# Performance work log

Hardware: AMD Instinct MI355X
Metric: run time of the kernel (lower is better)

The kernel has to match this reference:

```python
import jax, jax.numpy as jnp
import numpy as np

B = 2; R_PER = 512; R = B * R_PER; RM_PER = 128; RM = B * RM_PER
NUM_CLASSES = 81; C = 256
IMG_H = 800.0; IMG_W = 800.0
SCALES = (0.25, 0.125, 0.0625, 0.03125)  # FPN strides 4,8,16,32
REG_W = (10.0, 10.0, 5.0, 5.0)
LOG_1000_16 = 4.135166556742356  # math.log(1000/16)


def _prep(c, size):
    # torchvision roi_align (aligned=False) coordinate handling
    valid = (c > -1.0) & (c < size)
    c = jnp.clip(c, 0.0, size - 1.0)
    lo = jnp.clip(jnp.floor(c), 0.0, size - 2.0).astype(jnp.int32)
    frac = c - lo.astype(c.dtype)
    return lo, frac, valid


def roi_align(feat, boxes, b_idx, scale, out_size, sr=2):
    # feat [B,C,H,W], boxes [R,4] in image coords, b_idx [R] int
    _, Cn, H, W = feat.shape
    bb = boxes * scale
    x1, y1 = bb[:, 0], bb[:, 1]
    rw = jnp.maximum(bb[:, 2] - x1, 1.0)
    rh = jnp.maximum(bb[:, 3] - y1, 1.0)
    n = out_size * sr
    g = (jnp.arange(n, dtype=feat.dtype) + 0.5) / (sr * out_size)
    ys = y1[:, None] + rh[:, None] * g[None, :]  # [R,n]
    xs = x1[:, None] + rw[:, None] * g[None, :]
    y0, ly, yv = _prep(ys, H)
    x0, lx, xv = _prep(xs, W)
    bi = b_idx[:, None, None]
    yy = y0[:, :, None]; xx = x0[:, None, :]
    f00 = feat[bi, :, yy, xx]          # [R,n,n,C]
    f01 = feat[bi, :, yy, xx + 1]
    f10 = feat[bi, :, yy + 1, xx]
    f11 = feat[bi, :, yy + 1, xx + 1]
    ly_ = ly[:, :, None, None]; lx_ = lx[:, None, :, None]
    v = (f00 * (1 - ly_) * (1 - lx_) + f01 * (1 - ly_) * lx_
         + f10 * ly_ * (1 - lx_) + f11 * ly_ * lx_)
    mask = (yv[:, :, None] & xv[:, None, :]).astype(v.dtype)[..., None]
    v = v * mask
    Rn = boxes.shape[0]
    v = v.reshape(Rn, out_size, sr, out_size, sr, Cn).mean(axis=(2, 4))
    return jnp.transpose(v, (0, 3, 1, 2))  # [R,C,out,out]


def multiscale_roi_align(feats, boxes, b_idx, out_size):
    area = jnp.maximum(boxes[:, 2] - boxes[:, 0], 0.0) * jnp.maximum(boxes[:, 3] - boxes[:, 1], 0.0)
    lvl = jnp.clip(jnp.floor(4.0 + jnp.log2(jnp.sqrt(area) / 224.0 + 1e-6)), 2.0, 5.0).astype(jnp.int32) - 2
    out = 0.0
    for i, (f, s) in enumerate(zip(feats, SCALES)):
        out = out + roi_align(f, boxes, b_idx, s, out_size) * (lvl == i)[:, None, None, None].astype(f.dtype)
    return out


def decode_boxes(deltas, boxes):
    # deltas [R,K,4], boxes [R,4]
    wx, wy, ww, wh = REG_W
    w = boxes[:, 2] - boxes[:, 0]; h = boxes[:, 3] - boxes[:, 1]
    cx = boxes[:, 0] + 0.5 * w; cy = boxes[:, 1] + 0.5 * h
    dx = deltas[..., 0] / wx; dy = deltas[..., 1] / wy
    dw = jnp.minimum(deltas[..., 2] / ww, LOG_1000_16)
    dh = jnp.minimum(deltas[..., 3] / wh, LOG_1000_16)
    pcx = dx * w[:, None] + cx[:, None]; pcy = dy * h[:, None] + cy[:, None]
    pw = jnp.exp(dw) * w[:, None]; ph = jnp.exp(dh) * h[:, None]
    out = jnp.stack([pcx - 0.5 * pw, pcy - 0.5 * ph, pcx + 0.5 * pw, pcy + 0.5 * ph], axis=-1)
    hi = jnp.array([IMG_W, IMG_H, IMG_W, IMG_H], dtype=out.dtype)
    return jnp.clip(out, 0.0, hi)  # process_box clip-to-image


def conv3x3(x, w, b):
    y = jax.lax.conv_general_dilated(x, w, (1, 1), ((1, 1), (1, 1)),
                                     dimension_numbers=('NCHW', 'OIHW', 'NCHW'))
    return jax.nn.relu(y + b[None, :, None, None])


def _forward(feat0, feat1, feat2, feat3, proposals, fc1_w, fc1_b, fc2_w, fc2_b,
             cls_w, cls_b, bbox_w, bbox_b, mconv_w, mconv_b, deconv_w, deconv_b,
             mlogit_w, mlogit_b, batch_idx):
    feats = (feat0, feat1, feat2, feat3)
    # box branch
    bf = multiscale_roi_align(feats, proposals, batch_idx, 7).reshape(R, -1)  # [R, 256*49]
    x = jax.nn.relu(bf @ fc1_w.T + fc1_b)
    x = jax.nn.relu(x @ fc2_w.T + fc2_b)
    scores = jax.nn.softmax(x @ cls_w.T + cls_b, axis=-1)          # [R,81]
    deltas = (x @ bbox_w.T + bbox_b).reshape(R, NUM_CLASSES, 4)
    boxes = decode_boxes(deltas, proposals)                        # [R,81,4]
    # mask branch on top-of-list detections (RM_PER per image), box at argmax fg class
    idx_m = jnp.concatenate([jnp.arange(RM_PER), R_PER + jnp.arange(RM_PER)])
    labels = jnp.argmax(scores[idx_m, 1:], axis=-1) + 1            # [RM]
    mboxes = boxes[idx_m, labels]                                  # [RM,4]
    mf = multiscale_roi_align(feats, mboxes, batch_idx[idx_m], 14)  # [RM,256,14,14]
    for i in range(4):
        mf = conv3x3(mf, mconv_w[i], mconv_b[i])
    # ConvTranspose2d k=2 s=2 (non-overlapping) as einsum, PyTorch IOHW weights
    t = jnp.einsum('bcij,copq->boipjq', mf, deconv_w).reshape(RM, C, 28, 28)
    t = jax.nn.relu(t + deconv_b[None, :, None, None])
    ml = jnp.einsum('bchw,oc->bohw', t, mlogit_w) + mlogit_b[None, :, None, None]
    masks = jax.nn.sigmoid(ml[jnp.arange(RM), labels])             # [RM,28,28]
    return scores, boxes, masks


def setup_inputs() -> dict:
    key = jax.random.key(0)
    ks = jax.random.split(key, 16)
    rn = lambda i, shape, s=1.0: jax.random.normal(ks[i], shape, dtype=jnp.float32) * s
    feat0 = rn(0, (B, C, 200, 200))
    feat1 = rn(1, (B, C, 100, 100))
    feat2 = rn(2, (B, C, 50, 50))
    feat3 = rn(3, (B, C, 25, 25))
    u = jax.random.uniform(ks[4], (R, 4), dtype=jnp.float32)
    x1 = u[:, 0] * (IMG_W - 64.0); y1 = u[:, 1] * (IMG_H - 64.0)
    w = 16.0 + u[:, 2] * 300.0; h = 16.0 + u[:, 3] * 300.0
    proposals = jnp.stack([x1, y1, jnp.minimum(x1 + w, IMG_W), jnp.minimum(y1 + h, IMG_H)], axis=1)
    batch_idx = jnp.repeat(jnp.arange(B, dtype=jnp.int32), R_PER)
    return dict(
        feat0=feat0, feat1=feat1, feat2=feat2, feat3=feat3,
        proposals=proposals,
        fc1_w=rn(5, (1024, C * 49), 0.01), fc1_b=jnp.zeros(1024, jnp.float32),
        fc2_w=rn(6, (1024, 1024), 0.02), fc2_b=jnp.zeros(1024, jnp.float32),
        cls_w=rn(7, (NUM_CLASSES, 1024), 0.02), cls_b=jnp.zeros(NUM_CLASSES, jnp.float32),
        bbox_w=rn(8, (NUM_CLASSES * 4, 1024), 0.01), bbox_b=jnp.zeros(NUM_CLASSES * 4, jnp.float32),
        mconv_w=rn(9, (4, C, C, 3, 3), 0.03), mconv_b=jnp.zeros((4, C), jnp.float32),
        deconv_w=rn(10, (C, C, 2, 2), 0.06), deconv_b=jnp.zeros(C, jnp.float32),
        mlogit_w=rn(11, (NUM_CLASSES, C), 0.06), mlogit_b=jnp.zeros(NUM_CLASSES, jnp.float32),
        batch_idx=batch_idx,
    )


def reference(feat0, feat1, feat2, feat3, proposals, fc1_w, fc1_b, fc2_w, fc2_b,
              cls_w, cls_b, bbox_w, bbox_b, mconv_w, mconv_b, deconv_w, deconv_b,
              mlogit_w, mlogit_b, batch_idx):
    return _forward(feat0, feat1, feat2, feat3, proposals, fc1_w, fc1_b, fc2_w, fc2_b,
                    cls_w, cls_b, bbox_w, bbox_b, mconv_w, mconv_b, deconv_w, deconv_b,
                    mlogit_w, mlogit_b, batch_idx)
```

## Files before the change

kernel.cpp:

```cpp
#include <hip/hip_runtime.h>


#define NUM_CLASSES 81
#define CDIM 256
#define RTOT 1024
#define RMASK 256
#define LOG1000_16 4.135166556742356f

typedef _Float16 half8v __attribute__((ext_vector_type(8)));
typedef _Float16 half4v __attribute__((ext_vector_type(4)));
typedef float    float4v __attribute__((ext_vector_type(4)));
typedef float    float2a4 __attribute__((ext_vector_type(2), aligned(4)));

__device__ __forceinline__ void gload_lds16(const void* g, void* l) {
    __builtin_amdgcn_global_load_lds(
        (const __attribute__((address_space(1))) void*)g,
        (__attribute__((address_space(3))) void*)l, 16, 0, 0);
}

__global__ __launch_bounds__(256) void transpose_nhwc_kernel(
    const float* __restrict__ in, float* __restrict__ out, int H, int W)
{
    __shared__ float tile[64][65];
    int t = threadIdx.x;
    int xl = t & 63, cq = t >> 6;
    int x0 = blockIdx.x * 64;
    int y  = blockIdx.y;
    int b  = blockIdx.z >> 2;
    int c0 = (blockIdx.z & 3) * 64;

    const float* ip = in + (((size_t)(b*CDIM + c0))*H + y)*W + x0;
    if (x0 + xl < W) {
        #pragma unroll
        for (int i = 0; i < 16; ++i) {
            int cl = cq + i*4;
            tile[cl][xl] = ip[(size_t)cl*H*W + xl];
        }
    }
    __syncthreads();
    float* op = out + (((size_t)b*H + y)*W + x0)*CDIM + c0;
    #pragma unroll
    for (int i = 0; i < 16; ++i) {
        int xw = cq + i*4;
        if (x0 + xw < W)
            op[(size_t)xw*CDIM + xl] = tile[xl][xw];
    }
}

__device__ __forceinline__ void axis_taps(
    float start, float ext, int o, float invn, int N,
    float* wgt, int* idx)
{
    #pragma unroll
    for (int s = 0; s < 2; ++s) {
        int i = o*2 + s;
        float g = ((float)i + 0.5f) * invn;
        float c = start + ext*g;
        float mv = ((c > -1.f) && (c < (float)N)) ? 1.f : 0.f;
        float cl = fminf(fmaxf(c, 0.f), (float)(N-1));
        int   i0 = (int)fminf(floorf(cl), (float)(N-2));
        float l  = cl - (float)i0;
        wgt[s*2+0] = (1.f-l)*mv;
        wgt[s*2+1] = l*mv;
        idx[s*2+0] = i0;
        idx[s*2+1] = i0+1;
    }
}

__global__ __launch_bounds__(256) void roi_align7_nhwc_kernel(
    const float* __restrict__ fT0, const float* __restrict__ fT1,
    const float* __restrict__ fT2, const float* __restrict__ fT3,
    const float* __restrict__ props, const int* __restrict__ bidx,
    _Float16* __restrict__ bf_h, _Float16* __restrict__ bf_l)
{
    __shared__ _Float16 lh[256*49];
    __shared__ _Float16 ll[256*49];
    int r = blockIdx.x, t = threadIdx.x;
    int lane = t & 63, wv = t >> 6;

    float x1 = props[r*4+0], y1 = props[r*4+1];
    float x2 = props[r*4+2], y2 = props[r*4+3];
    float area = fmaxf(x2-x1, 0.f) * fmaxf(y2-y1, 0.f);
    float lf = floorf(4.f + log2f(sqrtf(area)/224.f + 1e-6f));
    lf = fminf(fmaxf(lf, 2.f), 5.f);
    int lvl = (int)lf - 2;

    const float* fT; int H, W; float scale;
    if (lvl == 0)      { fT = fT0; H = 200; W = 200; scale = 0.25f; }
    else if (lvl == 1) { fT = fT1; H = 100; W = 100; scale = 0.125f; }
    else if (lvl == 2) { fT = fT2; H = 50;  W = 50;  scale = 0.0625f; }
    else               { fT = fT3; H = 25;  W = 25;  scale = 0.03125f; }
    int b = bidx[r];
    const float* fb = fT + ((size_t)b*H*W)*CDIM + lane*4;

    float x1s = x1*scale, y1s = y1*scale;
    float rw = fmaxf(x2*scale - x1s, 1.f);
    float rh = fmaxf(y2*scale - y1s, 1.f);

    for (int p = wv; p < 49; p += 4) {
        int oy = p / 7, ox = p % 7;
        float uy[4]; int yr[4];
        axis_taps(y1s, rh, oy, 1.f/14.f, H, uy, yr);
        float wx[4]; int xc[4];
        axis_taps(x1s, rw, ox, 1.f/14.f, W, wx, xc);

        float a0 = 0.f, a1 = 0.f, a2 = 0.f, a3 = 0.f;
        #pragma unroll
        for (int a = 0; a < 4; ++a) {
            const float* rowp = fb + (size_t)(yr[a]*W)*CDIM;
            #pragma unroll
            for (int c2 = 0; c2 < 4; ++c2) {
                float w = uy[a]*wx[c2];
                float4v v = *(const float4v*)(rowp + xc[c2]*CDIM);
                a0 += w*v[0]; a1 += w*v[1]; a2 += w*v[2]; a3 += w*v[3];
            }
        }
        float av[4] = {a0, a1, a2, a3};
        #pragma unroll
        for (int e = 0; e < 4; ++e) {
            float vv = av[e]*0.25f;
            _Float16 h = (_Float16)vv;
            int c = lane*4 + e;
            lh[c*49 + p] = h;
            ll[c*49 + p] = (_Float16)((vv - (float)h)*2048.f);
        }
    }
    __syncthreads();
    size_t ob = (size_t)r*12544;
    for (int k = t; k < 12544; k += 256) {
        bf_h[ob + k] = lh[k];
        bf_l[ob + k] = ll[k];
    }
}

__global__ __launch_bounds__(256) void roi_align14_nhwc_kernel(
    const float* __restrict__ fT0, const float* __restrict__ fT1,
    const float* __restrict__ fT2, const float* __restrict__ fT3,
    const float* __restrict__ mboxes, const int* __restrict__ bidx,
    _Float16* __restrict__ outT)
{
    int mi = blockIdx.x, py = blockIdx.y;
    int t = threadIdx.x;
    int lane = t & 63, wv = t >> 6;

    float x1 = mboxes[mi*4+0], y1 = mboxes[mi*4+1];
    float x2 = mboxes[mi*4+2], y2 = mboxes[mi*4+3];
    float area = fmaxf(x2-x1, 0.f) * fmaxf(y2-y1, 0.f);
    float lf = floorf(4.f + log2f(sqrtf(area)/224.f + 1e-6f));
    lf = fminf(fmaxf(lf, 2.f), 5.f);
    int lvl = (int)lf - 2;

    const float* fT; int H, W; float scale;
    if (lvl == 0)      { fT = fT0; H = 200; W = 200; scale = 0.25f; }
    else if (lvl == 1) { fT = fT1; H = 100; W = 100; scale = 0.125f; }
    else if (lvl == 2) { fT = fT2; H = 50;  W = 50;  scale = 0.0625f; }
    else               { fT = fT3; H = 25;  W = 25;  scale = 0.03125f; }
    int ridx = (mi < 128) ? mi : mi + 384;
    int b = bidx[ridx];
    const float* fb = fT + ((size_t)b*H*W)*CDIM + lane*4;

    float x1s = x1*scale, y1s = y1*scale;
    float rw = fmaxf(x2*scale - x1s, 1.f);
    float rh = fmaxf(y2*scale - y1s, 1.f);

    for (int pp = wv; pp < 49; pp += 4) {
        int p = py*49 + pp;
        int oy = p / 14, ox = p % 14;
        float uy[4]; int yr[4];
        axis_taps(y1s, rh, oy, 1.f/28.f, H, uy, yr);
        float wx[4]; int xc[4];
        axis_taps(x1s, rw, ox, 1.f/28.f, W, wx, xc);

        float a0 = 0.f, a1 = 0.f, a2 = 0.f, a3 = 0.f;
        #pragma unroll
        for (int a = 0; a < 4; ++a) {
            const float* rowp = fb + (size_t)(yr[a]*W)*CDIM;
            #pragma unroll
            for (int c2 = 0; c2 < 4; ++c2) {
                float w = uy[a]*wx[c2];
                float4v v = *(const float4v*)(rowp + xc[c2]*CDIM);
                a0 += w*v[0]; a1 += w*v[1]; a2 += w*v[2]; a3 += w*v[3];
            }
        }
        half4v hv;
        hv[0] = (_Float16)(a0*0.25f);
        hv[1] = (_Float16)(a1*0.25f);
        hv[2] = (_Float16)(a2*0.25f);
        hv[3] = (_Float16)(a3*0.25f);
        *(half4v*)(outT + ((size_t)mi*196 + p)*CDIM + lane*4) = hv;
    }
}

__global__ __launch_bounds__(256) void roi_align7_kernel(
    const float* __restrict__ f0, const float* __restrict__ f1,
    const float* __restrict__ f2, const float* __restrict__ f3,
    const float* __restrict__ props, const int* __restrict__ bidx,
    _Float16* __restrict__ bf_h, _Float16* __restrict__ bf_l)
{
    int r  = blockIdx.x;
    int cg = blockIdx.y;
    int t = threadIdx.x;
    if (t >= 196) return;
    int p  = t % 49;
    int cl = t / 49;
    int oy = p / 7, ox = p % 7;

    float x1 = props[r*4+0], y1 = props[r*4+1];
    float x2 = props[r*4+2], y2 = props[r*4+3];
    float area = fmaxf(x2-x1, 0.f) * fmaxf(y2-y1, 0.f);
    float lf = floorf(4.f + log2f(sqrtf(area)/224.f + 1e-6f));
    lf = fminf(fmaxf(lf, 2.f), 5.f);
    int lvl = (int)lf - 2;

    const float* feat; int H, W; float scale;
    if (lvl == 0)      { feat = f0; H = 200; W = 200; scale = 0.25f; }
    else if (lvl == 1) { feat = f1; H = 100; W = 100; scale = 0.125f; }
    else if (lvl == 2) { feat = f2; H = 50;  W = 50;  scale = 0.0625f; }
    else               { feat = f3; H = 25;  W = 25;  scale = 0.03125f; }
    int b = bidx[r];

    float x1s = x1*scale, y1s = y1*scale;
    float rw = fmaxf(x2*scale - x1s, 1.f);
    float rh = fmaxf(y2*scale - y1s, 1.f);

    int   offs[4];
    float w00[4], w01[4], w10[4], w11[4];
    #pragma unroll
    for (int sy = 0; sy < 2; ++sy) {
        int iy = oy*2 + sy;
        float gy = ((float)iy + 0.5f) / 14.f;
        float yc = y1s + rh*gy;
        bool  yv = (yc > -1.f) && (yc < (float)H);
        float ycl = fminf(fmaxf(yc, 0.f), (float)(H-1));
        int   y0  = (int)fminf(floorf(ycl), (float)(H-2));
        float ly  = ycl - (float)y0;
        #pragma unroll
        for (int sx = 0; sx < 2; ++sx) {
            int ix = ox*2 + sx;
            float gx = ((float)ix + 0.5f) / 14.f;
            float xc = x1s + rw*gx;
            bool  xv = (xc > -1.f) && (xc < (float)W);
            float xcl = fminf(fmaxf(xc, 0.f), (float)(W-1));
            int   x0  = (int)fminf(floorf(xcl), (float)(W-2));
            float lx  = xcl - (float)x0;
            float m = (yv && xv) ? 1.f : 0.f;
            int s = sy*2 + sx;
            offs[s] = y0*W + x0;
            w00[s] = (1.f-ly)*(1.f-lx)*m;
            w01[s] = (1.f-ly)*lx*m;
            w10[s] = ly*(1.f-lx)*m;
            w11[s] = ly*lx*m;
        }
    }

    size_t HW = (size_t)H * W;
    #pragma unroll 4
    for (int k = 0; k < 16; ++k) {
        int c = cg*64 + cl + k*4;
        const float* fb = feat + ((size_t)b*CDIM + c) * HW;
        float acc = 0.f;
        #pragma unroll
        for (int s = 0; s < 4; ++s) {
            const float* q = fb + offs[s];
            float2a4 u = *(const float2a4*)q;
            float2a4 v = *(const float2a4*)(q + W);
            acc += w00[s]*u.x + w01[s]*u.y + w10[s]*v.x + w11[s]*v.y;
        }
        float v = acc * 0.25f;
        _Float16 h = (_Float16)v;
        size_t o = (size_t)r*12544 + c*49 + p;
        bf_h[o] = h;
        bf_l[o] = (_Float16)((v - (float)h) * 2048.f);
    }
}

template<int BMODE>
__global__ __launch_bounds__(256, 2) void gemm_fc2(
    const _Float16* __restrict__ Ah, const _Float16* __restrict__ Al,
    const float* __restrict__ B32,
    const _Float16* __restrict__ Bh16, const _Float16* __restrict__ Bl16,
    float* __restrict__ Cp, int K, int KS, int NS)
{
    __shared__ __align__(16) char smem[2*32768];

    int t = threadIdx.x;
    int lane = t & 63, wave = t >> 6;
    int wm = wave >> 1, wn = wave & 1;
    int ln = lane & 15, q = lane >> 4;

    int gx = gridDim.x, gy = gridDim.y;
    int lin = blockIdx.x + gx*(blockIdx.y + gy*blockIdx.z);
    int per = (gx*gy*(int)gridDim.z) >> 3;
    int nl  = (lin & 7)*per + (lin >> 3);
    int bn  = nl % gx;
    int tmp = nl / gx;
    int bm  = tmp % gy;
    int kz  = tmp / gy;

    size_t kbase = (size_t)kz * KS;
    int asub = lane >> 2;
    int achk = (lane & 3) ^ ((lane >> 3) & 3);

    const _Float16* Agh0 = Ah + (size_t)(bm*128 + wave*32 + asub)*K + kbase + achk*8;
    const _Float16* Agh1 = Agh0 + (size_t)16*K;
    const _Float16* Agl0 = Al + (size_t)(bm*128 + wave*32 + asub)*K + kbase + achk*8;
    const _Float16* Agl1 = Agl0 + (size_t)16*K;
    int adst0 = (wave*32 + 0)*32;
    int adst1 = (wave*32 + 16)*32;

    const _Float16 *Bgh0=nullptr, *Bgh1=nullptr, *Bgl0=nullptr, *Bgl1=nullptr;
    const float *Bg0=nullptr, *Bg1=nullptr, *Bg2=nullptr, *Bg3=nullptr;
    int fdst0 = 0;
    if constexpr (BMODE == 1) {
        Bgh0 = Bh16 + (size_t)(bn*128 + wave*32 + asub)*K + kbase + achk*8;
        Bgh1 = Bgh0 + (size_t)16*K;
        Bgl0 = Bl16 + (size_t)(bn*128 + wave*32 + asub)*K + kbase + achk*8;
        Bgl1 = Bgl0 + (size_t)16*K;
    } else {
        int br8  = lane >> 3;
        int bchk = (lane & 7) ^ br8;
        const float* base = B32 + (size_t)(bn*128 + wave*32 + br8)*K + kbase + bchk*4;
        Bg0 = base;
        Bg1 = base + (size_t)8*K;
        Bg2 = base + (size_t)16*K;
        Bg3 = base + (size_t)24*K;
        fdst0 = (wave*32)*32;
    }

    auto AhB = [&](int b){ return (_Float16*)(smem + b*32768); };
    auto AlB = [&](int b){ return (_Float16*)(smem + b*32768 + 8192); };
    auto BhB = [&](int b){ return (_Float16*)(smem + b*32768 + 16384); };
    auto BlB = [&](int b){ return (_Float16*)(smem + b*32768 + 24576); };
    auto BfB = [&](int b){ return (float*)   (smem + b*32768 + 16384); };

    auto dma = [&](int k0, int b) {
        gload_lds16(Agh0 + k0, AhB(b) + adst0);
        gload_lds16(Agh1 + k0, AhB(b) + adst1);
        gload_lds16(Agl0 + k0, AlB(b) + adst0);
        gload_lds16(Agl1 + k0, AlB(b) + adst1);
        if constexpr (BMODE == 1) {
            gload_lds16(Bgh0 + k0, BhB(b) + adst0);
            gload_lds16(Bgh1 + k0, BhB(b) + adst1);
            gload_lds16(Bgl0 + k0, BlB(b) + adst0);
            gload_lds16(Bgl1 + k0, BlB(b) + adst1);
        } else {
            gload_lds16(Bg0 + k0, BfB(b) + fdst0);
            gload_lds16(Bg1 + k0, BfB(b) + fdst0 + 8*32);
            gload_lds16(Bg2 + k0, BfB(b) + fdst0 + 16*32);
            gload_lds16(Bg3 + k0, BfB(b) + fdst0 + 24*32);
        }
    };

    float4v acc1[4][4], acc2[4][4];
    #pragma unroll
    for (int i = 0; i < 4; ++i)
        #pragma unroll
        for (int j = 0; j < 4; ++j) {
            acc1[i][j] = (float4v){0.f,0.f,0.f,0.f};
            acc2[i][j] = (float4v){0.f,0.f,0.f,0.f};
        }

    int cq = (q ^ ((ln >> 1) & 3)) * 8;

    auto compute = [&](int b) {
        const _Float16* ah = AhB(b);
        const _Float16* al = AlB(b);
        half8v afh[4], afl[4], bfh[4], bfl[4];
        #pragma unroll
        for (int i = 0; i < 4; ++i) {
            int ra = (wm*64 + i*16 + ln)*32 + cq;
            afh[i] = *(const half8v*)&ah[ra];
            afl[i] = *(const half8v*)&al[ra];
        }
        if constexpr (BMODE == 1) {
            const _Float16* bh = BhB(b);
            const _Float16* bl = BlB(b);
            #pragma unroll
            for (int j = 0; j < 4; ++j) {
                int rb = (wn*64 + j*16 + ln)*32 + cq;
                bfh[j] = *(const half8v*)&bh[rb];
                bfl[j] = *(const half8v*)&bl[rb];
            }
        } else {
            const float* bfp = BfB(b);
            #pragma unroll
            for (int j = 0; j < 4; ++j) {
                int row = wn*64 + j*16 + ln;
                int c0 = (q*2)   ^ (row & 7);
                int c1 = (q*2+1) ^ (row & 7);
                float4v f0 = *(const float4v*)&bfp[row*32 + c0*4];
                float4v f1 = *(const float4v*)&bfp[row*32 + c1*4];
                #pragma unroll
                for (int e = 0; e < 4; ++e) {
                    _Float16 h0 = (_Float16)f0[e];
                    bfh[j][e] = h0;
                    bfl[j][e] = (_Float16)((f0[e] - (float)h0) * 2048.f);
                    _Float16 h1 = (_Float16)f1[e];
                    bfh[j][4+e] = h1;
                    bfl[j][4+e] = (_Float16)((f1[e] - (float)h1) * 2048.f);
                }
            }
        }
        #pragma unroll
        for (int i = 0; i < 4; ++i) {
            #pragma unroll
            for (int j = 0; j < 4; ++j) {
                acc1[i][j] = __builtin_amdgcn_mfma_f32_16x16x32_f16(
                    afh[i], bfh[j], acc1[i][j], 0, 0, 0);
                acc2[i][j] = __builtin_amdgcn_mfma_f32_16x16x32_f16(
                    afh[i], bfl[j], acc2[i][j], 0, 0, 0);
                acc2[i][j] = __builtin_amdgcn_mfma_f32_16x16x32_f16(
                    afl[i], bfh[j], acc2[i][j], 0, 0, 0);
            }
        }
    };

    int NT = KS / 32;
    dma(0, 0);
    if (NT > 1) dma(32, 1);

    for (int tt = 0; tt < NT; ++tt) {
        if (tt < NT-1) asm volatile("s_waitcnt vmcnt(8)" ::: "memory");
        else           asm volatile("s_waitcnt vmcnt(0)" ::: "memory");
        __builtin_amdgcn_s_barrier();
        asm volatile("" ::: "memory");
        compute(tt & 1);
        asm volatile("" ::: "memory");
        __builtin_amdgcn_s_barrier();
        if (tt + 2 < NT) dma((tt+2)*32, tt & 1);
    }

    float* Cpz = Cp + (size_t)kz*1024*NS;
    #pragma unroll
    for (int i = 0; i < 4; ++i) {
        #pragma unroll
        for (int j = 0; j < 4; ++j) {
            int col = bn*128 + wn*64 + j*16 + ln;
            #pragma unroll
            for (int reg = 0; reg < 4; ++reg) {
                int row = bm*128 + wm*64 + i*16 + q*4 + reg;
                Cpz[(size_t)row*NS + col] =
                    acc1[i][j][reg] + acc2[i][j][reg] * (1.f/2048.f);
            }
        }
    }
}

__global__ __launch_bounds__(256) void fc_reduce_kernel(
    const float* __restrict__ Cp, const float* __restrict__ bias,
    float* __restrict__ out, _Float16* __restrict__ outh,
    _Float16* __restrict__ outl, int nparts, int ns4, int do_relu)
{
    int i = blockIdx.x*256 + threadIdx.x;
    const float4* p = (const float4*)Cp;
    int pstride = 1024*ns4;
    float sx = 0.f, sy = 0.f, sz = 0.f, sw = 0.f;
    for (int j = 0; j < nparts; ++j) {
        float4 s = p[i + j*pstride];
        sx += s.x; sy += s.y; sz += s.z; sw += s.w;
    }
    float4 b4 = ((const float4*)bias)[i & (ns4-1)];
    float4 v;
    v.x = sx + b4.x; v.y = sy + b4.y; v.z = sz + b4.z; v.w = sw + b4.w;
    if (do_relu) {
        v.x = fmaxf(v.x, 0.f); v.y = fmaxf(v.y, 0.f);
        v.z = fmaxf(v.z, 0.f); v.w = fmaxf(v.w, 0.f);
    }
    if (out) ((float4*)out)[i] = v;
    if (outh) {
        float vv[4] = {v.x, v.y, v.z, v.w};
        half4v hh, hl;
        #pragma unroll
        for (int c2 = 0; c2 < 4; ++c2) {
            _Float16 h = (_Float16)vv[c2];
            hh[c2] = h;
            hl[c2] = (_Float16)((vv[c2] - (float)h) * 2048.f);
        }
        ((half4v*)outh)[i] = hh;
        ((half4v*)outl)[i] = hl;
    }
}

__global__ __launch_bounds__(256) void repack_split_kernel(
    const float* __restrict__ w, _Float16* __restrict__ h,
    _Float16* __restrict__ l)
{
    int i = blockIdx.x*256 + threadIdx.x;
    float4 v = ((const float4*)w)[i];
    float vv[4] = {v.x, v.y, v.z, v.w};
    half4v hh, hl;
    #pragma unroll
    for (int c2 = 0; c2 < 4; ++c2) {
        _Float16 hj = (_Float16)vv[c2];
        hh[c2] = hj;
        hl[c2] = (_Float16)((vv[c2] - (float)hj) * 2048.f);
    }
    ((half4v*)h)[i] = hh;
    ((half4v*)l)[i] = hl;
}

__global__ __launch_bounds__(256) void repack_head_kernel(
    const float* __restrict__ cls_w, const float* __restrict__ cls_b,
    const float* __restrict__ bbox_w, const float* __restrict__ bbox_b,
    _Float16* __restrict__ Wcat_h, _Float16* __restrict__ Wcat_l,
    float* __restrict__ bcat)
{
    int i = blockIdx.x*256 + threadIdx.x;
    int row = i >> 10, col = i & 1023;
    float v = 0.f;
    if (row < 81) v = cls_w[row*1024 + col];
    else if (row < 405) v = bbox_w[(row-81)*1024 + col];
    _Float16 h = (_Float16)v;
    Wcat_h[i] = h;
    Wcat_l[i] = (_Float16)((v - (float)h) * 2048.f);
    if (i < 512) {
        float bv = 0.f;
        if (i < 81) bv = cls_b[i];
        else if (i < 405) bv = bbox_b[i-81];
        bcat[i] = bv;
    }
}

__global__ __launch_bounds__(128) void heads_finish_kernel(
    const float* __restrict__ L, const float* __restrict__ props,
    float* __restrict__ scores, float* __restrict__ boxes,
    int* __restrict__ labels, float* __restrict__ mboxes)
{
    __shared__ float lg[NUM_CLASSES];
    __shared__ float red[2];
    __shared__ int slab;
    int r = blockIdx.x, t = threadIdx.x;
    const float* Lr = L + (size_t)r*512;
    if (t < NUM_CLASSES) lg[t] = Lr[t];
    __syncthreads();
    if (t == 0) {
        float mx = lg[0];
        for (int j = 1; j < NUM_CLASSES; ++j) mx = fmaxf(mx, lg[j]);
        red[0] = mx;
    }
    __syncthreads();
    float mx = red[0];
    if (t < NUM_CLASSES) lg[t] = expf(lg[t] - mx);
    __syncthreads();
    if (t == 0) {
        float s = 0.f;
        int best = 1; float bv = lg[1];
        for (int j = 0; j < NUM_CLASSES; ++j) {
            s += lg[j];
            if (j >= 1 && lg[j] > bv) { bv = lg[j]; best = j; }
        }
        red[1] = 1.f/s;
        slab = best;
    }
    __syncthreads();
    if (t < NUM_CLASSES) scores[(size_t)r*NUM_CLASSES + t] = lg[t]*red[1];

    bool sel = (r < 128) || (r >= 512 && r < 640);
    int mi = (r < 128) ? r : r - 384;
    if (t == 0 && sel) labels[mi] = slab;

    if (t < NUM_CLASSES) {
        float px1 = props[r*4+0], py1 = props[r*4+1];
        float px2 = props[r*4+2], py2 = props[r*4+3];
        float pw = px2 - px1, ph = py2 - py1;
        float cx = px1 + 0.5f*pw, cy = py1 + 0.5f*ph;
        const float* dl = Lr + 81 + t*4;
        float d0 = dl[0] * 0.1f;
        float d1 = dl[1] * 0.1f;
        float d2 = fminf(dl[2] * 0.2f, LOG1000_16);
        float d3 = fminf(dl[3] * 0.2f, LOG1000_16);
        float pcx = d0*pw + cx, pcy = d1*ph + cy;
        float qw = expf(d2)*pw, qh = expf(d3)*ph;
        float b0 = fminf(fmaxf(pcx - 0.5f*qw, 0.f), 800.f);
        float b1 = fminf(fmaxf(pcy - 0.5f*qh, 0.f), 800.f);
        float b2 = fminf(fmaxf(pcx + 0.5f*qw, 0.f), 800.f);
        float b3 = fminf(fmaxf(pcy + 0.5f*qh, 0.f), 800.f);
        size_t ob = ((size_t)r*NUM_CLASSES + t)*4;
        boxes[ob+0] = b0; boxes[ob+1] = b1; boxes[ob+2] = b2; boxes[ob+3] = b3;
        if (sel && t == slab) {
            mboxes[mi*4+0] = b0; mboxes[mi*4+1] = b1;
            mboxes[mi*4+2] = b2; mboxes[mi*4+3] = b3;
        }
    }
}

__global__ __launch_bounds__(256) void roi_align14_kernel(
    const float* __restrict__ f0, const float* __restrict__ f1,
    const float* __restrict__ f2, const float* __restrict__ f3,
    const float* __restrict__ mboxes, const int* __restrict__ bidx,
    _Float16* __restrict__ outT)
{
    int mi = blockIdx.x;
    int cg = blockIdx.y;
    int t = threadIdx.x;
    if (t >= 196) return;
    int oy = t / 14, ox = t % 14;

    float x1 = mboxes[mi*4+0], y1 = mboxes[mi*4+1];
    float x2 = mboxes[mi*4+2], y2 = mboxes[mi*4+3];
    float area = fmaxf(x2-x1, 0.f) * fmaxf(y2-y1, 0.f);
    float lf = floorf(4.f + log2f(sqrtf(area)/224.f + 1e-6f));
    lf = fminf(fmaxf(lf, 2.f), 5.f);
    int lvl = (int)lf - 2;

    const float* feat; int H, W; float scale;
    if (lvl == 0)      { feat = f0; H = 200; W = 200; scale = 0.25f; }
    else if (lvl == 1) { feat = f1; H = 100; W = 100; scale = 0.125f; }
    else if (lvl == 2) { feat = f2; H = 50;  W = 50;  scale = 0.0625f; }
    else               { feat = f3; H = 25;  W = 25;  scale = 0.03125f; }
    int ridx = (mi < 128) ? mi : mi + 384;
    int b = bidx[ridx];

    float x1s = x1*scale, y1s = y1*scale;
    float rw = fmaxf(x2*scale - x1s, 1.f);
    float rh = fmaxf(y2*scale - y1s, 1.f);

    int   offs[4];
    float w00[4], w01[4], w10[4], w11[4];
    #pragma unroll
    for (int sy = 0; sy < 2; ++sy) {
        int iy = oy*2 + sy;
        float gy = ((float)iy + 0.5f) / 28.f;
        float yc = y1s + rh*gy;
        bool  yv = (yc > -1.f) && (yc < (float)H);
        float ycl = fminf(fmaxf(yc, 0.f), (float)(H-1));
        int   y0  = (int)fminf(floorf(ycl), (float)(H-2));
        float ly  = ycl - (float)y0;
        #pragma unroll
        for (int sx = 0; sx < 2; ++sx) {
            int ix = ox*2 + sx;
            float gx = ((float)ix + 0.5f) / 28.f;
            float xc = x1s + rw*gx;
            bool  xv = (xc > -1.f) && (xc < (float)W);
            float xcl = fminf(fmaxf(xc, 0.f), (float)(W-1));
            int   x0  = (int)fminf(floorf(xcl), (float)(W-2));
            float lx  = xcl - (float)x0;
            float m = (yv && xv) ? 1.f : 0.f;
            int s = sy*2 + sx;
            offs[s] = y0*W + x0;
            w00[s] = (1.f-ly)*(1.f-lx)*m;
            w01[s] = (1.f-ly)*lx*m;
            w10[s] = ly*(1.f-lx)*m;
            w11[s] = ly*lx*m;
        }
    }

    size_t HW = (size_t)H * W;
    _Float16* orow = outT + ((size_t)mi*196 + t)*CDIM + cg*32;
    const float* fbase = feat + ((size_t)b*CDIM + cg*32) * HW;
    #pragma unroll
    for (int c8 = 0; c8 < 32; c8 += 8) {
        half8v hv;
        #pragma unroll
        for (int cc = 0; cc < 8; ++cc) {
            const float* fb = fbase + (size_t)(c8+cc) * HW;
            float acc = 0.f;
            #pragma unroll
            for (int s = 0; s < 4; ++s) {
                const float* q = fb + offs[s];
                float2a4 u = *(const float2a4*)q;
                float2a4 v = *(const float2a4*)(q + W);
                acc += w00[s]*u.x + w01[s]*u.y + w10[s]*v.x + w11[s]*v.y;
            }
            hv[cc] = (_Float16)(acc * 0.25f);
        }
        *(half8v*)(orow + c8) = hv;
    }
}

__global__ __launch_bounds__(256) void repack_wts_kernel(
    const float* __restrict__ w, _Float16* __restrict__ Wr)
{
    int i = blockIdx.x*256 + threadIdx.x;
    int ci = i & 255;
    int rest = i >> 8;
    int co = rest & 255;
    int rest2 = rest >> 8;
    int tap = rest2 % 9;
    int l = rest2 / 9;
    Wr[i] = (_Float16)w[(((size_t)(l*256 + co)*256 + ci)*9) + tap];
}

__global__ __launch_bounds__(256) void repack_dw_kernel(
    const float* __restrict__ dw, _Float16* __restrict__ Wd)
{
    int i = blockIdx.x*256 + threadIdx.x;
    int n = i >> 8, k = i & 255;
    Wd[i] = (_Float16)dw[(size_t)k*1024 + n];
}

#define PSTR 40

__global__ __launch_bounds__(256, 2) void conv3x3_mfma_kernel(
    const _Float16* __restrict__ inT, const _Float16* __restrict__ Wr,
    const float* __restrict__ bias, _Float16* __restrict__ outT, int layer)
{
    __shared__ _Float16 lin[256*PSTR];

    int t = threadIdx.x;
    int lane = t & 63;
    int wave = t >> 6;
    int ln = lane & 15;
    int q  = lane >> 4;
    int q8 = q*8;
    int r  = blockIdx.x >> 1;
    int bc = blockIdx.x & 1;
    int co_w = bc*128 + wave*32;

    const _Float16* WrL = Wr + (size_t)layer*9*256*256;
    const _Float16* inR = inT + (size_t)r*196*256;

    for (int i = t; i < 256*PSTR; i += 256) lin[i] = (_Float16)0.f;

    float4v acc[13][2];
    #pragma unroll
    for (int nt = 0; nt < 13; ++nt) {
        acc[nt][0] = (float4v){0.f,0.f,0.f,0.f};
        acc[nt][1] = (float4v){0.f,0.f,0.f,0.f};
    }

    for (int ci0 = 0; ci0 < 256; ci0 += 32) {
        __syncthreads();
        for (int idx = t; idx < 784; idx += 256) {
            int p = idx >> 2, g = idx & 3;
            float4 v = *(const float4*)(inR + (size_t)p*256 + ci0 + g*8);
            int row = (p*37450) >> 19;
            int col = p - row*14;
            *(float4*)&lin[((row+1)*16 + (col+1))*PSTR + g*8] = v;
        }
        __syncthreads();

        half8v aw[9][2];
        #pragma unroll
        for (int tap = 0; tap < 9; ++tap) {
            #pragma unroll
            for (int u = 0; u < 2; ++u)
                aw[tap][u] = *(const half8v*)(
                    WrL + ((size_t)tap*256 + co_w + u*16 + ln)*256 + ci0 + q8);
        }

        #pragma unroll
        for (int nt = 0; nt < 13; ++nt) {
            int n = nt*16 + ln;
            int row = (n*37450) >> 19;
            int col = n - row*14;
            int pb = (n < 196) ? (row*16 + col) : 0;
            const _Float16* bp = &lin[pb*PSTR + q8];
            #pragma unroll
            for (int ky = 0; ky < 3; ++ky) {
                #pragma unroll
                for (int kx = 0; kx < 3; ++kx) {
                    half8v bv = *(const half8v*)(bp + (ky*16 + kx)*PSTR);
                    acc[nt][0] = __builtin_amdgcn_mfma_f32_16x16x32_f16(
                        aw[ky*3+kx][0], bv, acc[nt][0], 0, 0, 0);
                    acc[nt][1] = __builtin_amdgcn_mfma_f32_16x16x32_f16(
                        aw[ky*3+kx][1], bv, acc[nt][1], 0, 0, 0);
                }
            }
        }
    }

    #pragma unroll
    for (int u = 0; u < 2; ++u) {
        float4 bi = *(const float4*)&bias[layer*256 + co_w + u*16 + q*4];
        float bia[4] = {bi.x, bi.y, bi.z, bi.w};
        #pragma unroll
        for (int nt = 0; nt < 13; ++nt) {
            int n = nt*16 + ln;
            if (n < 196) {
                half4v hv;
                #pragma unroll
                for (int i = 0; i < 4; ++i)
                    hv[i] = (_Float16)fmaxf(acc[nt][u][i] + bia[i], 0.f);
                *(half4v*)(outT + ((size_t)r*196 + n)*256 + co_w + u*16 + q*4) = hv;
            }
        }
    }
}

#define DSTR 264

template<int NMT>
__device__ __forceinline__ void deconv_pass(
    const _Float16* actL, const _Float16* __restrict__ Wd,
    const float* __restrict__ db, const float* __restrict__ mlw,
    int lab, float (*sred)[4], int wv, int ln, int q, int px0)
{
    float P[NMT][4];
    #pragma unroll
    for (int mt = 0; mt < NMT; ++mt)
        #pragma unroll
        for (int r2 = 0; r2 < 4; ++r2) P[mt][r2] = 0.f;

    for (int c = 0; c < 8; ++c) {
        int n0 = wv*256 + c*32;
        float4v acc[NMT][2];
        #pragma unroll
        for (int mt = 0; mt < NMT; ++mt) {
            acc[mt][0] = (float4v){0.f,0.f,0.f,0.f};
            acc[mt][1] = (float4v){0.f,0.f,0.f,0.f};
        }
        #pragma unroll
        for (int k = 0; k < 8; ++k) {
            const _Float16* wp = Wd + ((size_t)(n0 + ln))*256 + k*32 + q*8;
            half8v b0 = *(const half8v*)wp;
            half8v b1 = *(const half8v*)(wp + 16*256);
            #pragma unroll
            for (int mt = 0; mt < NMT; ++mt) {
                half8v a = *(const half8v*)&actL[(mt*16 + ln)*DSTR + k*32 + q*8];
                acc[mt][0] = __builtin_amdgcn_mfma_f32_16x16x32_f16(
                    a, b0, acc[mt][0], 0, 0, 0);
                acc[mt][1] = __builtin_amdgcn_mfma_f32_16x16x32_f16(
                    a, b1, acc[mt][1], 0, 0, 0);
            }
        }
        #pragma unroll
        for (int j = 0; j < 2; ++j) {
            int n = n0 + j*16 + ln;
            int o = n >> 2;
            float bo = db[o];
            float wl = mlw[lab*256 + o];
            #pragma unroll
            for (int mt = 0; mt < NMT; ++mt)
                #pragma unroll
                for (int r2 = 0; r2 < 4; ++r2)
                    P[mt][r2] += fmaxf(acc[mt][j][r2] + bo, 0.f) * wl;
        }
    }
    #pragma unroll
    for (int mt = 0; mt < NMT; ++mt)
        #pragma unroll
        for (int r2 = 0; r2 < 4; ++r2) {
            float v = P[mt][r2];
            v += __shfl_xor(v, 4);
            v += __shfl_xor(v, 8);
            int px = px0 + mt*16 + q*4 + r2;
            if (ln < 4 && px < 196) atomicAdd(&sred[px][ln], v);
        }
}

__global__ __launch_bounds__(256, 1) void deconv_mask_mfma_kernel(
    const _Float16* __restrict__ mfT, const _Float16* __restrict__ Wd,
    const float* __restrict__ db, const float* __restrict__ mlw,
    const float* __restrict__ mlb, const int* __restrict__ labels,
    float* __restrict__ masks)
{
    __shared__ _Float16 act[112*DSTR];
    __shared__ float sred[196][4];
    int t = threadIdx.x;
    int lane = t & 63, wv = t >> 6, ln = lane & 15, q = lane >> 4;
    int mi = blockIdx.x;
    int lab = labels[mi];

    for (int i = t; i < 784; i += 256) ((float*)sred)[i] = 0.f;

    for (int idx = t; idx < 112*32; idx += 256) {
        int px = idx >> 5, g = idx & 31;
        *(float4*)&act[px*DSTR + g*8] =
            *(const float4*)(mfT + ((size_t)mi*196 + px)*256 + g*8);
    }
    __syncthreads();
    deconv_pass<7>(act, Wd, db, mlw, lab, sred, wv, ln, q, 0);
    __syncthreads();

    for (int idx = t; idx < 84*32; idx += 256) {
        int px = idx >> 5, g = idx & 31;
        *(float4*)&act[px*DSTR + g*8] =
            *(const float4*)(mfT + ((size_t)mi*196 + 112 + px)*256 + g*8);
    }
    __syncthreads();
    deconv_pass<6>(act, Wd, db, mlw, lab, sred, wv, ln, q, 112);
    __syncthreads();

    if (t < 196) {
        float bl = mlb[lab];
        int i2 = t / 14, j2 = t % 14;
        #pragma unroll
        for (int pq = 0; pq < 4; ++pq) {
            float s = sred[t][pq] + bl;
            int h = 2*i2 + (pq >> 1), w2 = 2*j2 + (pq & 1);
            masks[(size_t)mi*784 + h*28 + w2] = 1.f/(1.f + expf(-s));
        }
    }
}

extern "C" void kernel_launch(void* const* d_in, const int* in_sizes, int n_in,
                              void* d_out, int out_size, void* d_ws, size_t ws_size,
                              hipStream_t stream) {
    const float* f0      = (const float*)d_in[0];
    const float* f1      = (const float*)d_in[1];
    const float* f2      = (const float*)d_in[2];
    const float* f3      = (const float*)d_in[3];
    const float* props   = (const float*)d_in[4];
    const float* fc1_w   = (const float*)d_in[5];
    const float* fc1_b   = (const float*)d_in[6];
    const float* fc2_w   = (const float*)d_in[7];
    const float* fc2_b   = (const float*)d_in[8];
    const float* cls_w   = (const float*)d_in[9];
    const float* cls_b   = (const float*)d_in[10];
    const float* bbox_w  = (const float*)d_in[11];
    const float* bbox_b  = (const float*)d_in[12];
    const float* mconv_w = (const float*)d_in[13];
    const float* mconv_b = (const float*)d_in[14];
    const float* dconv_w = (const float*)d_in[15];
    const float* dconv_b = (const float*)d_in[16];
    const float* mlog_w  = (const float*)d_in[17];
    const float* mlog_b  = (const float*)d_in[18];
    const int*   bidx    = (const int*)d_in[19];

    char* wsb = (char*)d_ws;
    _Float16* bf_h = (_Float16*)wsb;
    _Float16* bf_l = (_Float16*)(wsb + 25690112);
    _Float16* fc2h = (_Float16*)wsb;
    _Float16* fc2l = (_Float16*)(wsb + 2097152);
    _Float16* bufA = (_Float16*)wsb;
    _Float16* bufB = (_Float16*)(wsb + 25690112);
    _Float16* x1h  = (_Float16*)(wsb + 51380224);
    _Float16* x1l  = (_Float16*)(wsb + 53477376);
    _Float16* x2h  = (_Float16*)(wsb + 55574528);
    _Float16* x2l  = (_Float16*)(wsb + 57671680);
    int*      labels = (int*)(wsb + 59768832);
    float*    mboxes = (float*)(wsb + 59772928);
    float*    Cp     = (float*)(wsb + 59781120);
    _Float16* Wr     = (_Float16*)(wsb + 59781120);
    _Float16* Wd     = (_Float16*)(wsb + 64499712);
    _Float16* Wcat_h = (_Float16*)(wsb + 76558336);
    _Float16* Wcat_l = (_Float16*)(wsb + 77606912);
    float*    bcat   = (float*)(wsb + 78655488);
    float*    Lh     = (float*)(wsb + 78659584);
    float*    fT0    = (float*)(wsb + 80756736);
    float*    fT1    = (float*)(wsb + 162676736);
    float*    fT2    = (float*)(wsb + 183156736);
    float*    fT3    = (float*)(wsb + 188276736);
    bool nhwc = (ws_size >= 189556736ull);
    _Float16* fc1wh  = (_Float16*)(wsb + 189556736);
    _Float16* fc1wl  = (_Float16*)(wsb + 215246848);
    bool fc1split = (ws_size >= 240936960ull);

    float* scores = (float*)d_out;
    float* boxes  = scores + RTOT*NUM_CLASSES;
    float* masks  = boxes + RTOT*NUM_CLASSES*4;

    if (nhwc) {
        transpose_nhwc_kernel<<<dim3(4, 200, 8), 256, 0, stream>>>(f0, fT0, 200, 200);
        transpose_nhwc_kernel<<<dim3(2, 100, 8), 256, 0, stream>>>(f1, fT1, 100, 100);
        transpose_nhwc_kernel<<<dim3(1,  50, 8), 256, 0, stream>>>(f2, fT2,  50,  50);
        transpose_nhwc_kernel<<<dim3(1,  25, 8), 256, 0, stream>>>(f3, fT3,  25,  25);
        roi_align7_nhwc_kernel<<<RTOT, 256, 0, stream>>>(
            fT0, fT1, fT2, fT3, props, bidx, bf_h, bf_l);
    } else {
        roi_align7_kernel<<<dim3(RTOT, 4), 256, 0, stream>>>(
            f0, f1, f2, f3, props, bidx, bf_h, bf_l);
    }

    repack_head_kernel<<<2048, 256, 0, stream>>>(cls_w, cls_b, bbox_w, bbox_b,
                                                 Wcat_h, Wcat_l, bcat);

    if (fc1split) {
        repack_split_kernel<<<12544, 256, 0, stream>>>(fc1_w, fc1wh, fc1wl);
        gemm_fc2<1><<<dim3(8, 8, 4), 256, 0, stream>>>(
            bf_h, bf_l, nullptr, fc1wh, fc1wl, Cp, 12544, 3136, 1024);
    } else {
        gemm_fc2<0><<<dim3(8, 8, 4), 256, 0, stream>>>(
            bf_h, bf_l, fc1_w, nullptr, nullptr, Cp, 12544, 3136, 1024);
    }
    fc_reduce_kernel<<<1024, 256, 0, stream>>>(Cp, fc1_b, nullptr, x1h, x1l,
                                               4, 256, 1);

    repack_split_kernel<<<1024, 256, 0, stream>>>(fc2_w, fc2h, fc2l);

    gemm_fc2<1><<<dim3(8, 8, 4), 256, 0, stream>>>(
        x1h, x1l, nullptr, fc2h, fc2l, Cp, 1024, 256, 1024);
    fc_reduce_kernel<<<1024, 256, 0, stream>>>(Cp, fc2_b, nullptr, x2h, x2l,
                                               4, 256, 1);

    gemm_fc2<1><<<dim3(4, 8, 8), 256, 0, stream>>>(
        x2h, x2l, nullptr, Wcat_h, Wcat_l, Cp, 1024, 128, 512);
    fc_reduce_kernel<<<512, 256, 0, stream>>>(Cp, bcat, Lh, nullptr, nullptr,
                                              8, 128, 0);

    heads_finish_kernel<<<RTOT, 128, 0, stream>>>(Lh, props, scores, boxes,
                                                  labels, mboxes);

    repack_wts_kernel<<<4*9*256, 256, 0, stream>>>(mconv_w, Wr);
    repack_dw_kernel<<<1024, 256, 0, stream>>>(dconv_w, Wd);

    if (nhwc) {
        roi_align14_nhwc_kernel<<<dim3(RMASK, 4), 256, 0, stream>>>(
            fT0, fT1, fT2, fT3, mboxes, bidx, bufA);
    } else {
        roi_align14_kernel<<<dim3(RMASK, 8), 256, 0, stream>>>(
            f0, f1, f2, f3, mboxes, bidx, bufA);
    }

    conv3x3_mfma_kernel<<<RMASK*2, 256, 0, stream>>>(bufA, Wr, mconv_b, bufB, 0);
    conv3x3_mfma_kernel<<<RMASK*2, 256, 0, stream>>>(bufB, Wr, mconv_b, bufA, 1);
    conv3x3_mfma_kernel<<<RMASK*2, 256, 0, stream>>>(bufA, Wr, mconv_b, bufB, 2);
    conv3x3_mfma_kernel<<<RMASK*2, 256, 0, stream>>>(bufB, Wr, mconv_b, bufA, 3);

    deconv_mask_mfma_kernel<<<RMASK, 256, 0, stream>>>(bufA, Wd, dconv_b, mlog_w,
                                                       mlog_b, labels, masks);
}
```

Measured before the change: 851.2 us.

## Use 8 waves per block in split-fp16 GEMM with 64x32 wave tiles

The split-precision MFMA GEMM block grows from 4 to 8 waves. Each wave now computes a 64x32 sub-tile instead of 64x64, and the global-to-LDS DMA is spread across 512 threads, so each thread issues half as many loads; the vmcnt wait drops to match. This halves accumulator registers per wave and raises the number of waves available to hide latency. In exchange, A fragments are reloaded from LDS by more waves, so LDS traffic per MFMA goes up.

```diff
diff --git a/kernel.cpp b/kernel.cpp
--- a/kernel.cpp
+++ b/kernel.cpp
@@ -275,7 +275,7 @@
 }
 
 template<int BMODE>
-__global__ __launch_bounds__(256, 2) void gemm_fc2(
+__global__ __launch_bounds__(512, 2) void gemm_fc2(
     const _Float16* __restrict__ Ah, const _Float16* __restrict__ Al,
     const float* __restrict__ B32,
     const _Float16* __restrict__ Bh16, const _Float16* __restrict__ Bl16,
@@ -285,7 +285,7 @@
 
     int t = threadIdx.x;
     int lane = t & 63, wave = t >> 6;
-    int wm = wave >> 1, wn = wave & 1;
+    int wm = wave >> 2, wn = wave & 3;
     int ln = lane & 15, q = lane >> 4;
 
     int gx = gridDim.x, gy = gridDim.y;
@@ -298,33 +298,25 @@
     int kz  = tmp / gy;
 
     size_t kbase = (size_t)kz * KS;
-    int asub = lane >> 2;
+    int arow = t >> 2;
     int achk = (lane & 3) ^ ((lane >> 3) & 3);
-
-    const _Float16* Agh0 = Ah + (size_t)(bm*128 + wave*32 + asub)*K + kbase + achk*8;
-    const _Float16* Agh1 = Agh0 + (size_t)16*K;
-    const _Float16* Agl0 = Al + (size_t)(bm*128 + wave*32 + asub)*K + kbase + achk*8;
-    const _Float16* Agl1 = Agl0 + (size_t)16*K;
-    int adst0 = (wave*32 + 0)*32;
-    int adst1 = (wave*32 + 16)*32;
-
-    const _Float16 *Bgh0=nullptr, *Bgh1=nullptr, *Bgl0=nullptr, *Bgl1=nullptr;
-    const float *Bg0=nullptr, *Bg1=nullptr, *Bg2=nullptr, *Bg3=nullptr;
-    int fdst0 = 0;
+    const _Float16* Agh = Ah + (size_t)(bm*128 + arow)*K + kbase + achk*8;
+    const _Float16* Agl = Al + (size_t)(bm*128 + arow)*K + kbase + achk*8;
+    int adst = wave * 512;
+
+    const _Float16 *Bgh = nullptr, *Bgl = nullptr;
+    const float *Bg0 = nullptr, *Bg1 = nullptr;
+    int bfdst0 = 0, bfdst1 = 0;
     if constexpr (BMODE == 1) {
-        Bgh0 = Bh16 + (size_t)(bn*128 + wave*32 + asub)*K + kbase + achk*8;
-        Bgh1 = Bgh0 + (size_t)16*K;
-        Bgl0 = Bl16 + (size_t)(bn*128 + wave*32 + asub)*K + kbase + achk*8;
-        Bgl1 = Bgl0 + (size_t)16*K;
+        Bgh = Bh16 + (size_t)(bn*128 + arow)*K + kbase + achk*8;
+        Bgl = Bl16 + (size_t)(bn*128 + arow)*K + kbase + achk*8;
     } else {
-        int br8  = lane >> 3;
-        int bchk = (lane & 7) ^ br8;
-        const float* base = B32 + (size_t)(bn*128 + wave*32 + br8)*K + kbase + bchk*4;
-        Bg0 = base;
-        Bg1 = base + (size_t)8*K;
-        Bg2 = base + (size_t)16*K;
-        Bg3 = base + (size_t)24*K;
-        fdst0 = (wave*32)*32;
+        int brow = t >> 3;
+        int bchk = (lane & 7) ^ ((lane >> 3) & 7);
+        Bg0 = B32 + (size_t)(bn*128 + brow)*K + kbase + bchk*4;
+        Bg1 = Bg0 + (size_t)64*K;
+        bfdst0 = wave*256;
+        bfdst1 = 2048 + wave*256;
     }
 
     auto AhB = [&](int b){ return (_Float16*)(smem + b*32768); };
@@ -334,28 +326,22 @@
     auto BfB = [&](int b){ return (float*)   (smem + b*32768 + 16384); };
 
     auto dma = [&](int k0, int b) {
-        gload_lds16(Agh0 + k0, AhB(b) + adst0);
-        gload_lds16(Agh1 + k0, AhB(b) + adst1);
-        gload_lds16(Agl0 + k0, AlB(b) + adst0);
-        gload_lds16(Agl1 + k0, AlB(b) + adst1);
+        gload_lds16(Agh + k0, AhB(b) + adst);
+        gload_lds16(Agl + k0, AlB(b) + adst);
         if constexpr (BMODE == 1) {
-            gload_lds16(Bgh0 + k0, BhB(b) + adst0);
-            gload_lds16(Bgh1 + k0, BhB(b) + adst1);
-            gload_lds16(Bgl0 + k0, BlB(b) + adst0);
-            gload_lds16(Bgl1 + k0, BlB(b) + adst1);
+            gload_lds16(Bgh + k0, BhB(b) + adst);
+            gload_lds16(Bgl + k0, BlB(b) + adst);
         } else {
-            gload_lds16(Bg0 + k0, BfB(b) + fdst0);
-            gload_lds16(Bg1 + k0, BfB(b) + fdst0 + 8*32);
-            gload_lds16(Bg2 + k0, BfB(b) + fdst0 + 16*32);
-            gload_lds16(Bg3 + k0, BfB(b) + fdst0 + 24*32);
+            gload_lds16(Bg0 + k0, BfB(b) + bfdst0);
+            gload_lds16(Bg1 + k0, BfB(b) + bfdst1);
         }
     };
 
-    float4v acc1[4][4], acc2[4][4];
+    float4v acc1[4][2], acc2[4][2];
     #pragma unroll
     for (int i = 0; i < 4; ++i)
         #pragma unroll
-        for (int j = 0; j < 4; ++j) {
+        for (int j = 0; j < 2; ++j) {
             acc1[i][j] = (float4v){0.f,0.f,0.f,0.f};
             acc2[i][j] = (float4v){0.f,0.f,0.f,0.f};
         }
@@ -365,7 +351,7 @@
     auto compute = [&](int b) {
         const _Float16* ah = AhB(b);
         const _Float16* al = AlB(b);
-        half8v afh[4], afl[4], bfh[4], bfl[4];
+        half8v afh[4], afl[4], bfh[2], bfl[2];
         #pragma unroll
         for (int i = 0; i < 4; ++i) {
             int ra = (wm*64 + i*16 + ln)*32 + cq;
@@ -376,16 +362,16 @@
             const _Float16* bh = BhB(b);
             const _Float16* bl = BlB(b);
             #pragma unroll
-            for (int j = 0; j < 4; ++j) {
-                int rb = (wn*64 + j*16 + ln)*32 + cq;
+            for (int j = 0; j < 2; ++j) {
+                int rb = (wn*32 + j*16 + ln)*32 + cq;
                 bfh[j] = *(const half8v*)&bh[rb];
                 bfl[j] = *(const half8v*)&bl[rb];
             }
         } else {
             const float* bfp = BfB(b);
             #pragma unroll
-            for (int j = 0; j < 4; ++j) {
-                int row = wn*64 + j*16 + ln;
+            for (int j = 0; j < 2; ++j) {
+                int row = wn*32 + j*16 + ln;
                 int c0 = (q*2)   ^ (row & 7);
                 int c1 = (q*2+1) ^ (row & 7);
                 float4v f0 = *(const float4v*)&bfp[row*32 + c0*4];
@@ -404,7 +390,7 @@
         #pragma unroll
         for (int i = 0; i < 4; ++i) {
             #pragma unroll
-            for (int j = 0; j < 4; ++j) {
+            for (int j = 0; j < 2; ++j) {
                 acc1[i][j] = __builtin_amdgcn_mfma_f32_16x16x32_f16(
                     afh[i], bfh[j], acc1[i][j], 0, 0, 0);
                 acc2[i][j] = __builtin_amdgcn_mfma_f32_16x16x32_f16(
@@ -420,7 +406,7 @@
     if (NT > 1) dma(32, 1);
 
     for (int tt = 0; tt < NT; ++tt) {
-        if (tt < NT-1) asm volatile("s_waitcnt vmcnt(8)" ::: "memory");
+        if (tt < NT-1) asm volatile("s_waitcnt vmcnt(4)" ::: "memory");
         else           asm volatile("s_waitcnt vmcnt(0)" ::: "memory");
         __builtin_amdgcn_s_barrier();
         asm volatile("" ::: "memory");
@@ -434,8 +420,8 @@
     #pragma unroll
     for (int i = 0; i < 4; ++i) {
         #pragma unroll
-        for (int j = 0; j < 4; ++j) {
-            int col = bn*128 + wn*64 + j*16 + ln;
+        for (int j = 0; j < 2; ++j) {
+            int col = bn*128 + wn*32 + j*16 + ln;
             #pragma unroll
             for (int reg = 0; reg < 4; ++reg) {
                 int row = bm*128 + wm*64 + i*16 + q*4 + reg;
@@ -958,10 +944,10 @@
 
     if (fc1split) {
         repack_split_kernel<<<12544, 256, 0, stream>>>(fc1_w, fc1wh, fc1wl);
-        gemm_fc2<1><<<dim3(8, 8, 4), 256, 0, stream>>>(
+        gemm_fc2<1><<<dim3(8, 8, 4), 512, 0, stream>>>(
             bf_h, bf_l, nullptr, fc1wh, fc1wl, Cp, 12544, 3136, 1024);
     } else {
-        gemm_fc2<0><<<dim3(8, 8, 4), 256, 0, stream>>>(
+        gemm_fc2<0><<<dim3(8, 8, 4), 512, 0, stream>>>(
             bf_h, bf_l, fc1_w, nullptr, nullptr, Cp, 12544, 3136, 1024);
     }
     fc_reduce_kernel<<<1024, 256, 0, stream>>>(Cp, fc1_b, nullptr, x1h, x1l,
@@ -969,12 +955,12 @@
 
     repack_split_kernel<<<1024, 256, 0, stream>>>(fc2_w, fc2h, fc2l);
 
-    gemm_fc2<1><<<dim3(8, 8, 4), 256, 0, stream>>>(
+    gemm_fc2<1><<<dim3(8, 8, 4), 512, 0, stream>>>(
         x1h, x1l, nullptr, fc2h, fc2l, Cp, 1024, 256, 1024);
     fc_reduce_kernel<<<1024, 256, 0, stream>>>(Cp, fc2_b, nullptr, x2h, x2l,
                                                4, 256, 1);
 
-    gemm_fc2<1><<<dim3(4, 8, 8), 256, 0, stream>>>(
+    gemm_fc2<1><<<dim3(4, 8, 8), 512, 0, stream>>>(
         x2h, x2l, nullptr, Wcat_h, Wcat_l, Cp, 1024, 128, 512);
     fc_reduce_kernel<<<512, 256, 0, stream>>>(Cp, bcat, Lh, nullptr, nullptr,
                                               8, 128, 0);
```

Measured after the change: 849.7 us. Within noise of the previous version (-0.2%).
